# Kernel tuning notes

Measured on AMD Instinct MI355X. Metric: run time of the kernel, lower is better.

Reference implementation:

```python
import jax, jax.numpy as jnp
import numpy as np

EMB_K = 512
EMB_DIM = 256
BETA = 0.25
GAMMA = 0.99
EPS = 1e-5
B, T = 16, 4096


def setup_inputs() -> dict:
    key = jax.random.key(0)
    k1, k2, k3 = jax.random.split(key, 3)
    return {
        "inputs": jax.random.normal(k1, (B, EMB_DIM, T), dtype=jnp.float32),
        "emb_weight": jax.random.normal(k2, (EMB_K, EMB_DIM), dtype=jnp.float32),
        "ema_w": jax.random.normal(k3, (EMB_K, EMB_DIM), dtype=jnp.float32),
        "ema_cluster_size": jnp.zeros((EMB_K,), dtype=jnp.float32),
    }


def reference(inputs, emb_weight, ema_w, ema_cluster_size):
    # [B, D, T] -> [B, T, D]
    x = jnp.transpose(inputs, (0, 2, 1))
    flat = x.reshape(-1, EMB_DIM)  # [N, D]

    # squared euclidean distances to codebook: [N, K]
    dist = (jnp.sum(flat * flat, axis=1, keepdims=True)
            + jnp.sum(emb_weight * emb_weight, axis=1)
            - 2.0 * flat @ emb_weight.T)
    idx = jnp.argmin(dist, axis=1)            # [N]
    enc = jax.nn.one_hot(idx, EMB_K, dtype=flat.dtype)  # [N, K]

    # --- EMA codebook update (training branch) ---
    counts = jax.ops.segment_sum(jnp.ones_like(idx, dtype=flat.dtype), idx,
                                 num_segments=EMB_K)  # == enc.sum(0)
    new_cs = ema_cluster_size * GAMMA + (1.0 - GAMMA) * counts
    n = jnp.sum(new_cs)
    new_cs = (new_cs + EPS) / (n + EMB_K * EPS) * n
    dw = jax.ops.segment_sum(flat, idx, num_segments=EMB_K)  # == enc.T @ flat
    new_ema_w = ema_w * GAMMA + (1.0 - GAMMA) * dw
    new_emb_weight = new_ema_w / new_cs[:, None]

    # quantize with updated codebook (gather == enc @ new_emb_weight)
    Q = new_emb_weight[idx].reshape(x.shape)  # [B, T, D]

    e_latent_loss = jnp.mean((jax.lax.stop_gradient(Q) - x) ** 2)
    loss = BETA * e_latent_loss

    # straight-through
    Q_st = x + jax.lax.stop_gradient(Q - x)

    avg_probs = jnp.mean(enc, axis=0)
    PP = jnp.exp(-jnp.sum(avg_probs * jnp.log(avg_probs + 1e-10)))

    return loss, jnp.transpose(Q_st, (0, 2, 1)), PP, enc
```

## Files before the change

### kernel.cpp

```cpp
#include <hip/hip_runtime.h>

#define N_TOT 65536
#define DIM 256
#define KK 512
#define TT 4096
#define BB 16

typedef short bf16x8 __attribute__((ext_vector_type(8)));
typedef float f32x4 __attribute__((ext_vector_type(4)));

__device__ __forceinline__ ushort f2bf(float f) {
    unsigned u = __float_as_uint(f);
    unsigned r = (u + 0x7fffu + ((u >> 16) & 1u)) >> 16;
    return (ushort)r;
}

__global__ void k_prep_e(const float* __restrict__ emb, float* __restrict__ se,
                         ushort* __restrict__ eb) {
    int k = blockIdx.x, tid = threadIdx.x;
    int c0 = tid * 4;
    float4 v = *(const float4*)(emb + k * DIM + c0);
    float f[4] = {v.x, v.y, v.z, v.w};
    float s = f[0] * f[0] + f[1] * f[1] + f[2] * f[2] + f[3] * f[3];
#pragma unroll
    for (int m = 1; m < 64; m <<= 1) s += __shfl_xor(s, m);
    if (tid == 0) se[k] = s;
    ushort h[4], l[4];
#pragma unroll
    for (int j = 0; j < 4; ++j) {
        h[j] = f2bf(f[j]);
        float hf = __uint_as_float(((unsigned)h[j]) << 16);
        l[j] = f2bf(f[j] - hf);
    }
    uint2 hp = make_uint2((unsigned)h[0] | ((unsigned)h[1] << 16),
                          (unsigned)h[2] | ((unsigned)h[3] << 16));
    uint2 lp = make_uint2((unsigned)l[0] | ((unsigned)l[1] << 16),
                          (unsigned)l[2] | ((unsigned)l[3] << 16));
    *(uint2*)(eb + (size_t)k * 512 + c0) = hp;
    *(uint2*)(eb + (size_t)k * 512 + 256 + c0) = lp;
}

__global__ __launch_bounds__(256) void k_split_x(const float* __restrict__ in,
                                                 ushort* __restrict__ xt) {
    __shared__ float ls[64][65];
    int tid = threadIdx.x;
    int b = blockIdx.x >> 8;
    int rest = blockIdx.x & 255;
    int tt = rest >> 2, dt = rest & 3;
    int t0 = tt * 64, d0 = dt * 64;
    int tl = tid & 63, dg = tid >> 6;
    const float* src = in + (size_t)b * DIM * TT + t0 + tl;
#pragma unroll
    for (int p = 0; p < 16; ++p) {
        int d = dg * 16 + p;
        ls[d][tl] = src[(size_t)(d0 + d) * TT];
    }
    __syncthreads();
    int c0 = dg * 16;
    int n = b * TT + t0 + tl;
    ushort* row = xt + (size_t)n * 512;
    ushort h[16], l[16];
#pragma unroll
    for (int j = 0; j < 16; ++j) {
        float v = ls[c0 + j][tl];
        h[j] = f2bf(v);
        float hf = __uint_as_float(((unsigned)h[j]) << 16);
        l[j] = f2bf(v - hf);
    }
    uint hu[8], lu[8];
#pragma unroll
    for (int j = 0; j < 8; ++j) {
        hu[j] = (unsigned)h[2 * j] | ((unsigned)h[2 * j + 1] << 16);
        lu[j] = (unsigned)l[2 * j] | ((unsigned)l[2 * j + 1] << 16);
    }
    *(uint4*)(row + d0 + c0) = make_uint4(hu[0], hu[1], hu[2], hu[3]);
    *(uint4*)(row + d0 + c0 + 8) = make_uint4(hu[4], hu[5], hu[6], hu[7]);
    *(uint4*)(row + 256 + d0 + c0) = make_uint4(lu[0], lu[1], lu[2], lu[3]);
    *(uint4*)(row + 256 + d0 + c0 + 8) = make_uint4(lu[4], lu[5], lu[6], lu[7]);
}

__global__ void k_zero(float* __restrict__ dw, unsigned* __restrict__ counts,
                       unsigned* __restrict__ lossd) {
    int i = blockIdx.x * 256 + threadIdx.x;
    if (i < 131072) dw[i] = 0.f;
    int j = i - 131072;
    if (j >= 0 && j < 512) counts[j] = 0u;
    if (j >= 512 && j < 514) lossd[j - 512] = 0u;
}

__global__ __launch_bounds__(128, 2) void k_dist(
    const ushort* __restrict__ xt, const ushort* __restrict__ eb,
    const float* __restrict__ se,
    float* __restrict__ partd, int* __restrict__ parti) {
    __shared__ ushort As[128 * 64];
    __shared__ ushort Bs[128 * 64];
    const int tid = threadIdx.x;
    const int lane = tid & 63, w = tid >> 6;
    const int id = blockIdx.x;
    const int lin = (id & 7) * 256 + (id >> 3);
    const int bj = lin & 3, bi = lin >> 2;
    const int n0 = bi * 128, k0 = bj * 128;

    f32x4 acc[8][4] = {};

    for (int it = 0; it < 12; ++it) {
        const int region = it >> 2, sub = it & 3;
        const int aoff = (region == 2 ? 256 : 0) + sub * 64;
        const int boff = (region == 1 ? 256 : 0) + sub * 64;
#pragma unroll
        for (int i = 0; i < 8; ++i) {
            int r = i * 16 + w * 8 + (lane >> 3);
            int slot = (lane & 7) ^ (r & 7);
            const ushort* ga = xt + (size_t)(n0 + r) * 512 + aoff + slot * 8;
            const ushort* gb = eb + (size_t)(k0 + r) * 512 + boff + slot * 8;
            __builtin_amdgcn_global_load_lds(
                (const __attribute__((address_space(1))) void*)ga,
                (__attribute__((address_space(3))) void*)&As[(i * 16 + w * 8) * 64],
                16, 0, 0);
            __builtin_amdgcn_global_load_lds(
                (const __attribute__((address_space(1))) void*)gb,
                (__attribute__((address_space(3))) void*)&Bs[(i * 16 + w * 8) * 64],
                16, 0, 0);
        }
        __syncthreads();
#pragma unroll
        for (int kk = 0; kk < 2; ++kk) {
            bf16x8 af[8], bfr[4];
#pragma unroll
            for (int mi = 0; mi < 8; ++mi) {
                int row = mi * 16 + (lane & 15);
                int slot = (kk * 4 + (lane >> 4)) ^ (row & 7);
                af[mi] = *(const bf16x8*)&As[row * 64 + slot * 8];
            }
#pragma unroll
            for (int ni = 0; ni < 4; ++ni) {
                int row = w * 64 + ni * 16 + (lane & 15);
                int slot = (kk * 4 + (lane >> 4)) ^ (row & 7);
                bfr[ni] = *(const bf16x8*)&Bs[row * 64 + slot * 8];
            }
#pragma unroll
            for (int mi = 0; mi < 8; ++mi)
#pragma unroll
                for (int ni = 0; ni < 4; ++ni)
                    acc[mi][ni] = __builtin_amdgcn_mfma_f32_16x16x32_bf16(
                        af[mi], bfr[ni], acc[mi][ni], 0, 0, 0);
        }
        __syncthreads();
    }

    float se4[4];
#pragma unroll
    for (int ni = 0; ni < 4; ++ni) se4[ni] = se[k0 + w * 64 + ni * 16 + (lane & 15)];
    float* pd = (float*)As;
    int* pi = (int*)Bs;
#pragma unroll
    for (int mi = 0; mi < 8; ++mi) {
#pragma unroll
        for (int j = 0; j < 4; ++j) {
            int r = mi * 16 + (lane >> 4) * 4 + j;
            float dmin = 3.4e38f;
            int bidx = 0x7fffffff;
#pragma unroll
            for (int ni = 0; ni < 4; ++ni) {
                int k = k0 + w * 64 + ni * 16 + (lane & 15);
                float dv = fmaf(-2.f, acc[mi][ni][j], se4[ni]);
                if (dv < dmin) { dmin = dv; bidx = k; }
            }
            pd[r * 32 + w * 16 + (lane & 15)] = dmin;
            pi[r * 32 + w * 16 + (lane & 15)] = bidx;
        }
    }
    __syncthreads();
    {
        float dmin = 3.4e38f;
        int bidx = 0x7fffffff;
        for (int c = 0; c < 32; ++c) {
            float dv = pd[tid * 32 + c];
            int iv = pi[tid * 32 + c];
            if (dv < dmin || (dv == dmin && iv < bidx)) { dmin = dv; bidx = iv; }
        }
        partd[(size_t)bj * N_TOT + n0 + tid] = dmin;
        parti[(size_t)bj * N_TOT + n0 + tid] = bidx;
    }
}

__global__ void k_combine(const float* __restrict__ partd, const int* __restrict__ parti,
                          int* __restrict__ idx, unsigned* __restrict__ counts) {
    __shared__ unsigned h[512];
    int tid = threadIdx.x;
    h[tid] = 0u;
    h[tid + 256] = 0u;
    __syncthreads();
    int n = blockIdx.x * 256 + tid;
    float dmin = 3.4e38f;
    int bidx = 0x7fffffff;
#pragma unroll
    for (int p = 0; p < 4; ++p) {
        float dv = partd[(size_t)p * N_TOT + n];
        int iv = parti[(size_t)p * N_TOT + n];
        if (dv < dmin || (dv == dmin && iv < bidx)) { dmin = dv; bidx = iv; }
    }
    idx[n] = bidx;
    atomicAdd(&h[bidx], 1u);
    __syncthreads();
    if (h[tid]) atomicAdd(&counts[tid], h[tid]);
    if (h[tid + 256]) atomicAdd(&counts[tid + 256], h[tid + 256]);
}

__global__ void k_enc_zero(float2* __restrict__ enc2) {
    size_t base = (size_t)blockIdx.x * (256 * 32) + threadIdx.x;
#pragma unroll
    for (int j = 0; j < 32; ++j) enc2[base + j * 256] = make_float2(0.f, 0.f);
}

__global__ void k_enc_ones(const int* __restrict__ idx, float* __restrict__ enc) {
    int n = blockIdx.x * 256 + threadIdx.x;
    enc[(size_t)n * KK + idx[n]] = 1.0f;
}

__global__ void k_scalars(const unsigned* __restrict__ counts, const float* __restrict__ cs_in,
                          float* __restrict__ csn, float* __restrict__ pp_out,
                          unsigned* __restrict__ cursor) {
    __shared__ float red[512];
    __shared__ unsigned sc[512];
    int k = threadIdx.x;
    unsigned ci = counts[k];
    float c = (float)ci;
    float pre = cs_in[k] * 0.99f + 0.01f * c;
    red[k] = pre;
    sc[k] = ci;
    __syncthreads();
#pragma unroll
    for (int s = 256; s > 0; s >>= 1) {
        if (k < s) red[k] += red[k + s];
        __syncthreads();
    }
    float nsum = red[0];
    __syncthreads();
    csn[k] = (pre + 1e-5f) / (nsum + 512 * 1e-5f) * nsum;
    float p = c * (1.0f / 65536.f);
    red[k] = -p * logf(p + 1e-10f);
    __syncthreads();
#pragma unroll
    for (int s = 256; s > 0; s >>= 1) {
        if (k < s) red[k] += red[k + s];
        __syncthreads();
    }
    if (k == 0) pp_out[0] = expf(red[0]);
#pragma unroll
    for (int s = 1; s < 512; s <<= 1) {
        unsigned v = (k >= s) ? sc[k - s] : 0u;
        __syncthreads();
        sc[k] += v;
        __syncthreads();
    }
    cursor[k] = sc[k] - ci;
}

__global__ void k_scatter(const int* __restrict__ idx, unsigned* __restrict__ cursor,
                          unsigned* __restrict__ sortedp) {
    int n = blockIdx.x * 256 + threadIdx.x;
    int k = idx[n];
    unsigned p = atomicAdd(&cursor[k], 1u);
    sortedp[p] = (unsigned)n | ((unsigned)k << 17);
}

__global__ __launch_bounds__(256) void k_dwsum(const ushort* __restrict__ xt,
                                               const unsigned* __restrict__ sortedp,
                                               float* __restrict__ dw) {
    int gw = blockIdx.x * 4 + (threadIdx.x >> 6);
    int lane = threadIdx.x & 63;
    int base = gw * 16;
    unsigned pk[16];
#pragma unroll
    for (int i = 0; i < 16; ++i) pk[i] = sortedp[base + i];
    float acc[8] = {0.f, 0.f, 0.f, 0.f, 0.f, 0.f, 0.f, 0.f};
    int curk = (int)(pk[0] >> 17);
#pragma unroll
    for (int i = 0; i < 16; ++i) {
        int n = (int)(pk[i] & 0x1ffffu);
        int k = (int)(pk[i] >> 17);
        if (k != curk) {
#pragma unroll
            for (int j = 0; j < 8; ++j) {
                float other = __shfl(acc[j], lane + 32);
                if (lane < 32) atomicAdd(&dw[curk * DIM + lane * 8 + j], acc[j] + other);
                acc[j] = 0.f;
            }
            curk = k;
        }
        uint4 v = *(const uint4*)(xt + (size_t)n * 512 + lane * 8);
        unsigned u[4] = {v.x, v.y, v.z, v.w};
#pragma unroll
        for (int j = 0; j < 4; ++j) {
            acc[2 * j] += __uint_as_float(u[j] << 16);
            acc[2 * j + 1] += __uint_as_float(u[j] & 0xffff0000u);
        }
    }
#pragma unroll
    for (int j = 0; j < 8; ++j) {
        float other = __shfl(acc[j], lane + 32);
        if (lane < 32) atomicAdd(&dw[curk * DIM + lane * 8 + j], acc[j] + other);
    }
}

__global__ void k_newemb(const float* __restrict__ ema_w, const float* __restrict__ dw,
                         const float* __restrict__ csn, float* __restrict__ newemb) {
    int i = blockIdx.x * 256 + threadIdx.x;
    int k = i >> 8;
    newemb[i] = (ema_w[i] * 0.99f + 0.01f * dw[i]) / csn[k];
}

__global__ __launch_bounds__(256) void k_out1(const float* __restrict__ in,
                                              const int* __restrict__ idx,
                                              const float* __restrict__ newemb,
                                              float* __restrict__ out1,
                                              unsigned long long* __restrict__ lossd) {
    __shared__ float q[256][68];
    __shared__ float redl[4];
    int tid = threadIdx.x;
    int b = blockIdx.x >> 6, tc = blockIdx.x & 63;
    int tl = tid & 63, dg = tid >> 6;
    int kk = idx[b * TT + tc * 64 + tl];
    const float4* ne4 = (const float4*)(newemb + (size_t)kk * DIM);
#pragma unroll
    for (int d4 = 0; d4 < 16; ++d4) {
        float4 v = ne4[dg * 16 + d4];
        int d = dg * 64 + d4 * 4;
        q[d + 0][tl] = v.x;
        q[d + 1][tl] = v.y;
        q[d + 2][tl] = v.z;
        q[d + 3][tl] = v.w;
    }
    __syncthreads();
    float lacc = 0.f;
    const float* xb = in + (size_t)b * DIM * TT + tc * 64;
    float* ob = out1 + (size_t)b * DIM * TT + tc * 64;
#pragma unroll 4
    for (int j = 0; j < 64; ++j) {
        int fi = tid + 256 * j;
        int d = fi >> 6, t = fi & 63;
        float qv = q[d][t];
        float xv = xb[(size_t)d * TT + t];
        ob[(size_t)d * TT + t] = qv;
        float df = qv - xv;
        lacc = fmaf(df, df, lacc);
    }
#pragma unroll
    for (int m = 1; m < 64; m <<= 1) lacc += __shfl_xor(lacc, m);
    if ((tid & 63) == 0) redl[tid >> 6] = lacc;
    __syncthreads();
    if (tid == 0) {
        double s = (double)redl[0] + (double)redl[1] + (double)redl[2] + (double)redl[3];
        atomicAdd((double*)lossd, s);
    }
}

__global__ void k_loss_fin(const double* __restrict__ lossd, float* __restrict__ out0) {
    out0[0] = (float)(0.25 * lossd[0] * (1.0 / 16777216.0));
}

extern "C" void kernel_launch(void* const* d_in, const int* in_sizes, int n_in,
                              void* d_out, int out_size, void* d_ws, size_t ws_size,
                              hipStream_t stream) {
    const float* in = (const float*)d_in[0];
    const float* emb = (const float*)d_in[1];
    const float* emaw = (const float*)d_in[2];
    const float* cs = (const float*)d_in[3];
    float* out = (float*)d_out;
    char* ws = (char*)d_ws;

    float* se = (float*)(ws + 0);
    float* partd = (float*)(ws + 264192);
    int* parti = (int*)(ws + 1312768);
    int* idx = (int*)(ws + 2361344);
    unsigned* counts = (unsigned*)(ws + 2623488);
    float* csn = (float*)(ws + 2625536);
    float* dw = (float*)(ws + 2627584);
    float* newemb = (float*)(ws + 3151872);
    double* lossd = (double*)(ws + 3676160);
    ushort* eb = (ushort*)(ws + 3676416);
    ushort* xt = (ushort*)(ws + 4200704);
    unsigned* sortedp = (unsigned*)(ws + 71309568);
    unsigned* cursor = (unsigned*)(ws + 71573760);

    float* out_loss = out;
    float* out_q = out + 1;
    float* out_pp = out + 16777217;
    float* enc = out + 16777218;

    hipLaunchKernelGGL(k_prep_e, dim3(512), dim3(64), 0, stream, emb, se, eb);
    hipLaunchKernelGGL(k_split_x, dim3(4096), dim3(256), 0, stream, in, xt);
    hipLaunchKernelGGL(k_zero, dim3(515), dim3(256), 0, stream, dw, counts, (unsigned*)lossd);
    hipLaunchKernelGGL(k_dist, dim3(2048), dim3(128), 0, stream, xt, eb, se, partd, parti);
    hipLaunchKernelGGL(k_combine, dim3(256), dim3(256), 0, stream, partd, parti, idx, counts);
    hipLaunchKernelGGL(k_enc_zero, dim3(2048), dim3(256), 0, stream, (float2*)enc);
    hipLaunchKernelGGL(k_enc_ones, dim3(256), dim3(256), 0, stream, idx, enc);
    hipLaunchKernelGGL(k_scalars, dim3(1), dim3(512), 0, stream, counts, cs, csn, out_pp, cursor);
    hipLaunchKernelGGL(k_scatter, dim3(256), dim3(256), 0, stream, idx, cursor, sortedp);
    hipLaunchKernelGGL(k_dwsum, dim3(1024), dim3(256), 0, stream, xt, sortedp, dw);
    hipLaunchKernelGGL(k_newemb, dim3(512), dim3(256), 0, stream, emaw, dw, csn, newemb);
    hipLaunchKernelGGL(k_out1, dim3(1024), dim3(256), 0, stream, in, idx, newemb, out_q,
                       (unsigned long long*)lossd);
    hipLaunchKernelGGL(k_loss_fin, dim3(1), dim3(1), 0, stream, lossd, out_loss);
}
```

Before: 349.0 us.

## Compute quantization loss algebraically instead of rereading inputs in output kernel

The loss sum of (q-x)^2 is expanded as sum x^2 + sum_k (count_k*|e_k|^2 - 2 dw_k·e_k). The x^2 part is accumulated in the transpose/split kernel, which already reads x, and the codebook part in k_newemb. k_out1 then no longer rereads the 64 MB input and only writes the quantized output. The expansion risks cancellation error in fp32 partial terms, although the sums are accumulated in double via atomics.

```diff
diff --git a/kernel.cpp b/kernel.cpp
--- a/kernel.cpp
+++ b/kernel.cpp
@@ -41,8 +41,10 @@
 }
 
 __global__ __launch_bounds__(256) void k_split_x(const float* __restrict__ in,
-                                                 ushort* __restrict__ xt) {
+                                                 ushort* __restrict__ xt,
+                                                 double* __restrict__ lossA) {
     __shared__ float ls[64][65];
+    __shared__ float r4[4];
     int tid = threadIdx.x;
     int b = blockIdx.x >> 8;
     int rest = blockIdx.x & 255;
@@ -50,11 +52,17 @@
     int t0 = tt * 64, d0 = dt * 64;
     int tl = tid & 63, dg = tid >> 6;
     const float* src = in + (size_t)b * DIM * TT + t0 + tl;
+    float ssq = 0.f;
 #pragma unroll
     for (int p = 0; p < 16; ++p) {
         int d = dg * 16 + p;
-        ls[d][tl] = src[(size_t)(d0 + d) * TT];
-    }
+        float v = src[(size_t)(d0 + d) * TT];
+        ls[d][tl] = v;
+        ssq = fmaf(v, v, ssq);
+    }
+#pragma unroll
+    for (int m = 1; m < 64; m <<= 1) ssq += __shfl_xor(ssq, m);
+    if (tl == 0) r4[dg] = ssq;
     __syncthreads();
     int c0 = dg * 16;
     int n = b * TT + t0 + tl;
@@ -77,6 +85,10 @@
     *(uint4*)(row + d0 + c0 + 8) = make_uint4(hu[4], hu[5], hu[6], hu[7]);
     *(uint4*)(row + 256 + d0 + c0) = make_uint4(lu[0], lu[1], lu[2], lu[3]);
     *(uint4*)(row + 256 + d0 + c0 + 8) = make_uint4(lu[4], lu[5], lu[6], lu[7]);
+    if (tid == 0) {
+        double s = (double)r4[0] + (double)r4[1] + (double)r4[2] + (double)r4[3];
+        atomicAdd(lossA, s);
+    }
 }
 
 __global__ void k_zero(float* __restrict__ dw, unsigned* __restrict__ counts,
@@ -85,7 +97,7 @@
     if (i < 131072) dw[i] = 0.f;
     int j = i - 131072;
     if (j >= 0 && j < 512) counts[j] = 0u;
-    if (j >= 512 && j < 514) lossd[j - 512] = 0u;
+    if (j >= 512 && j < 516) lossd[j - 512] = 0u;
 }
 
 __global__ __launch_bounds__(128, 2) void k_dist(
@@ -305,19 +317,24 @@
 }
 
 __global__ void k_newemb(const float* __restrict__ ema_w, const float* __restrict__ dw,
-                         const float* __restrict__ csn, float* __restrict__ newemb) {
+                         const float* __restrict__ csn, const unsigned* __restrict__ counts,
+                         float* __restrict__ newemb, double* __restrict__ lossB) {
     int i = blockIdx.x * 256 + threadIdx.x;
     int k = i >> 8;
-    newemb[i] = (ema_w[i] * 0.99f + 0.01f * dw[i]) / csn[k];
-}
-
-__global__ __launch_bounds__(256) void k_out1(const float* __restrict__ in,
-                                              const int* __restrict__ idx,
+    float dwv = dw[i];
+    float ne = (ema_w[i] * 0.99f + 0.01f * dwv) / csn[k];
+    newemb[i] = ne;
+    float c = (float)counts[k];
+    float term = fmaf(c * ne, ne, -2.f * dwv * ne);
+#pragma unroll
+    for (int m = 1; m < 64; m <<= 1) term += __shfl_xor(term, m);
+    if ((threadIdx.x & 63) == 0) atomicAdd(lossB, (double)term);
+}
+
+__global__ __launch_bounds__(256) void k_out1(const int* __restrict__ idx,
                                               const float* __restrict__ newemb,
-                                              float* __restrict__ out1,
-                                              unsigned long long* __restrict__ lossd) {
+                                              float* __restrict__ out1) {
     __shared__ float q[256][68];
-    __shared__ float redl[4];
     int tid = threadIdx.x;
     int b = blockIdx.x >> 6, tc = blockIdx.x & 63;
     int tl = tid & 63, dg = tid >> 6;
@@ -333,31 +350,17 @@
         q[d + 3][tl] = v.w;
     }
     __syncthreads();
-    float lacc = 0.f;
-    const float* xb = in + (size_t)b * DIM * TT + tc * 64;
     float* ob = out1 + (size_t)b * DIM * TT + tc * 64;
-#pragma unroll 4
+#pragma unroll 8
     for (int j = 0; j < 64; ++j) {
         int fi = tid + 256 * j;
         int d = fi >> 6, t = fi & 63;
-        float qv = q[d][t];
-        float xv = xb[(size_t)d * TT + t];
-        ob[(size_t)d * TT + t] = qv;
-        float df = qv - xv;
-        lacc = fmaf(df, df, lacc);
-    }
-#pragma unroll
-    for (int m = 1; m < 64; m <<= 1) lacc += __shfl_xor(lacc, m);
-    if ((tid & 63) == 0) redl[tid >> 6] = lacc;
-    __syncthreads();
-    if (tid == 0) {
-        double s = (double)redl[0] + (double)redl[1] + (double)redl[2] + (double)redl[3];
-        atomicAdd((double*)lossd, s);
+        ob[(size_t)d * TT + t] = q[d][t];
     }
 }
 
 __global__ void k_loss_fin(const double* __restrict__ lossd, float* __restrict__ out0) {
-    out0[0] = (float)(0.25 * lossd[0] * (1.0 / 16777216.0));
+    out0[0] = (float)(0.25 * (lossd[0] + lossd[1]) * (1.0 / 16777216.0));
 }
 
 extern "C" void kernel_launch(void* const* d_in, const int* in_sizes, int n_in,
@@ -390,8 +393,8 @@
     float* enc = out + 16777218;
 
     hipLaunchKernelGGL(k_prep_e, dim3(512), dim3(64), 0, stream, emb, se, eb);
-    hipLaunchKernelGGL(k_split_x, dim3(4096), dim3(256), 0, stream, in, xt);
     hipLaunchKernelGGL(k_zero, dim3(515), dim3(256), 0, stream, dw, counts, (unsigned*)lossd);
+    hipLaunchKernelGGL(k_split_x, dim3(4096), dim3(256), 0, stream, in, xt, lossd);
     hipLaunchKernelGGL(k_dist, dim3(2048), dim3(128), 0, stream, xt, eb, se, partd, parti);
     hipLaunchKernelGGL(k_combine, dim3(256), dim3(256), 0, stream, partd, parti, idx, counts);
     hipLaunchKernelGGL(k_enc_zero, dim3(2048), dim3(256), 0, stream, (float2*)enc);
@@ -399,8 +402,8 @@
     hipLaunchKernelGGL(k_scalars, dim3(1), dim3(512), 0, stream, counts, cs, csn, out_pp, cursor);
     hipLaunchKernelGGL(k_scatter, dim3(256), dim3(256), 0, stream, idx, cursor, sortedp);
     hipLaunchKernelGGL(k_dwsum, dim3(1024), dim3(256), 0, stream, xt, sortedp, dw);
-    hipLaunchKernelGGL(k_newemb, dim3(512), dim3(256), 0, stream, emaw, dw, csn, newemb);
-    hipLaunchKernelGGL(k_out1, dim3(1024), dim3(256), 0, stream, in, idx, newemb, out_q,
-                       (unsigned long long*)lossd);
+    hipLaunchKernelGGL(k_newemb, dim3(512), dim3(256), 0, stream, emaw, dw, csn, counts,
+                       newemb, lossd + 1);
+    hipLaunchKernelGGL(k_out1, dim3(1024), dim3(256), 0, stream, idx, newemb, out_q);
     hipLaunchKernelGGL(k_loss_fin, dim3(1), dim3(1), 0, stream, lossd, out_loss);
 }
```

New measurement: 374.8 us. 1.07x slower.
